# Optimization experiments

Hardware: AMD Instinct MI355X
Metric: run time of the kernel (lower is better)

The kernel has to match this reference:

```python
import jax, jax.numpy as jnp
import numpy as np

BIG = 1e30  # finite stand-in for +inf to keep grads clean


def _chamfer_loss(bin_center, ground_truth):
    # bin_center: [B, n_bins, 1] 1-D 'point cloud' of bin centers
    # ground_truth: [B, 1, H, W] depth map
    B = bin_center.shape[0]
    c = bin_center[..., 0]                      # [B, nb]
    p = ground_truth.reshape(B, -1)             # [B, V] flattened depth points
    mask = p >= 0.001                           # valid (non-near-zero) depths
    n = jnp.sum(mask, axis=1)                   # [B] valid count per sample
    Lmax = jnp.max(n)                           # pad_sequence pads every sample to L_max
    npad = (Lmax - n).astype(c.dtype)           # number of zero pad-points per sample

    # pairwise squared distances between bin centers and depth points
    D = (c[:, :, None] - p[:, None, :]) ** 2    # [B, nb, V]

    # direction 1: gt points -> nearest bin center (sum over points)
    dmin_p = jnp.min(D, axis=1)                 # [B, V]
    sumA = jnp.sum(jnp.where(mask, dmin_p, 0.0), axis=1)
    # each zero pad-point contributes min_j c_j^2
    c2 = c ** 2                                 # [B, nb]
    sumA = sumA + npad * jnp.min(c2, axis=1)

    # direction 2: bin centers -> nearest gt point (incl. zero pad-points if any)
    Dm = jnp.where(mask[:, None, :], D, jnp.asarray(BIG, D.dtype))
    min_valid = jnp.min(Dm, axis=2)             # [B, nb] min over valid points
    has_pad = (npad > 0)[:, None]
    min_b = jnp.where(has_pad, jnp.minimum(min_valid, c2), min_valid)
    sumB = jnp.sum(min_b, axis=1)               # [B]

    # chamferdist: point_reduction=sum, batch_reduction=mean, bidirectional
    return jnp.mean(sumA + sumB)


def setup_inputs() -> dict:
    key = jax.random.key(0)
    k1, k2 = jax.random.split(key)
    bin_center = jax.random.uniform(k1, (4, 256, 1), dtype=jnp.float32)
    ground_truth = jax.random.uniform(k2, (4, 1, 352, 448), dtype=jnp.float32)
    return {"bin_center": bin_center, "ground_truth": ground_truth}


def reference(bin_center, ground_truth):
    return _chamfer_loss(bin_center, ground_truth)
```

## Files before the change

### kernel.cpp

```cpp
#include <hip/hip_runtime.h>

#define NB   256
#define TPB  256
#define NI   (NB + 1)
#define G    128
#define MINF 1e30f
#define CAPD 1e15f

__global__ __launch_bounds__(NB) void k_sort(const float* __restrict__ bc,
                                             float* __restrict__ sbins,
                                             unsigned* __restrict__ gmin,
                                             unsigned* __restrict__ gmax) {
    __shared__ float s[NB];
    const int tid = threadIdx.x, b = blockIdx.x;
    s[tid] = bc[b * NB + tid];
    for (int t = tid; t < NI; t += NB) {
        gmin[b * NI + t] = 0xFFFFFFFFu;
        gmax[b * NI + t] = 0u;
    }
    __syncthreads();
    for (int k = 2; k <= NB; k <<= 1)
        for (int j = k >> 1; j > 0; j >>= 1) {
            const int ixj = tid ^ j;
            if (ixj > tid) {
                const float a = s[tid], bv = s[ixj];
                if ((a > bv) == ((tid & k) == 0)) { s[tid] = bv; s[ixj] = a; }
            }
            __syncthreads();
        }
    sbins[b * NB + tid] = s[tid];
}

__global__ __launch_bounds__(TPB) void k_main(
    const float* __restrict__ sbins, const float* __restrict__ gt,
    int V, int CH,
    float* __restrict__ sumA_part, int* __restrict__ cnt_part,
    unsigned* __restrict__ gmin, unsigned* __restrict__ gmax)
{
    const int b   = blockIdx.x / G;
    const int blk = blockIdx.x % G;
    const int tid = threadIdx.x;
    const int start = blk * CH;
    const int cn = min(CH, V - start);
    const float* __restrict__ gp = gt + (size_t)b * V + start;

    __shared__ float    c[NB];
    __shared__ unsigned imn[NI], imx[NI];
    c[tid] = sbins[b * NB + tid];
    for (int t = tid; t < NI; t += TPB) { imn[t] = 0xFFFFFFFFu; imx[t] = 0u; }
    __syncthreads();

    float sum = 0.f; int cnt = 0;
    for (int i = tid; i < cn; i += TPB) {
        const float q = gp[i];
        if (q >= 0.001f) {
            int idx = 0;
            #pragma unroll
            for (int st = 128; st >= 1; st >>= 1)
                idx += (c[idx + st - 1] <= q) ? st : 0;
            idx += (c[idx] <= q) ? 1 : 0;
            const float dlo = (idx > 0)  ? (q - c[idx - 1]) : MINF;
            const float dhi = (idx < NB) ? (c[idx] - q)     : MINF;
            const float d = fminf(dlo, dhi);
            sum += d * d; ++cnt;
            atomicMin(&imn[idx], __float_as_uint(q));
            atomicMax(&imx[idx], __float_as_uint(q));
        }
    }
    __syncthreads();

    for (int t = tid; t < NI; t += TPB) {
        const unsigned lo = imn[t], hi = imx[t];
        if (lo != 0xFFFFFFFFu) atomicMin(&gmin[b * NI + t], lo);
        if (hi != 0u)          atomicMax(&gmax[b * NI + t], hi);
    }

    for (int off = 32; off; off >>= 1) {
        sum += __shfl_down(sum, off);
        cnt += __shfl_down(cnt, off);
    }
    __shared__ float r4[4]; __shared__ int i4[4];
    if ((tid & 63) == 0) { r4[tid >> 6] = sum; i4[tid >> 6] = cnt; }
    __syncthreads();
    if (tid == 0) {
        sumA_part[blockIdx.x] = r4[0] + r4[1] + r4[2] + r4[3];
        cnt_part [blockIdx.x] = i4[0] + i4[1] + i4[2] + i4[3];
    }
}

__global__ __launch_bounds__(TPB) void k_final(
    const float* __restrict__ sbins,
    const float* __restrict__ sumA_part, const int* __restrict__ cnt_part,
    const unsigned* __restrict__ gmin, const unsigned* __restrict__ gmax,
    int B, float* __restrict__ out)
{
    const int tid = threadIdx.x;
    __shared__ float pm[NB], sm[NB];
    __shared__ float r4[4]; __shared__ int i4[4]; __shared__ float q4[4];
    __shared__ float ssa[8]; __shared__ int sn[8];

    for (int bb = 0; bb < B; ++bb) {
        float s = 0.f; int cc = 0;
        for (int k = tid; k < G; k += TPB) {
            s  += sumA_part[bb * G + k];
            cc += cnt_part [bb * G + k];
        }
        for (int off = 32; off; off >>= 1) { s += __shfl_down(s, off); cc += __shfl_down(cc, off); }
        if ((tid & 63) == 0) { r4[tid >> 6] = s; i4[tid >> 6] = cc; }
        __syncthreads();
        if (tid == 0) { ssa[bb] = r4[0]+r4[1]+r4[2]+r4[3]; sn[bb] = i4[0]+i4[1]+i4[2]+i4[3]; }
        __syncthreads();
    }
    int Lmax = 0;
    for (int bb = 0; bb < B; ++bb) Lmax = max(Lmax, sn[bb]);

    float total = 0.f;
    for (int bb = 0; bb < B; ++bb) {
        const unsigned hib = gmax[bb * NI + tid];
        const unsigned lob = gmin[bb * NI + tid + 1];
        pm[tid] = (hib == 0u)          ? -MINF : __uint_as_float(hib);
        sm[tid] = (lob == 0xFFFFFFFFu) ?  MINF : __uint_as_float(lob);
        __syncthreads();
        for (int off = 1; off < NB; off <<= 1) {
            const float vp = pm[tid], vs = sm[tid];
            const float op = (tid >= off)     ? pm[tid - off] : -MINF;
            const float os = (tid + off < NB) ? sm[tid + off] :  MINF;
            __syncthreads();
            pm[tid] = fmaxf(vp, op);
            sm[tid] = fminf(vs, os);
            __syncthreads();
        }
        const float cj = sbins[bb * NB + tid];
        const float c2 = cj * cj;
        const float d  = fminf(fminf(cj - pm[tid], sm[tid] - cj), CAPD);
        float bm = d * d;
        const int npad = Lmax - sn[bb];
        if (npad > 0) bm = fminf(bm, c2);
        float s = bm, mc = c2;
        for (int off = 32; off; off >>= 1) {
            s  += __shfl_down(s, off);
            mc  = fminf(mc, __shfl_down(mc, off));
        }
        if ((tid & 63) == 0) { r4[tid >> 6] = s; q4[tid >> 6] = mc; }
        __syncthreads();
        if (tid == 0)
            total += ssa[bb]
                   + (float)npad * fminf(fminf(q4[0], q4[1]), fminf(q4[2], q4[3]))
                   + (r4[0] + r4[1] + r4[2] + r4[3]);
        __syncthreads();
    }
    if (tid == 0) out[0] = total / (float)B;
}

extern "C" void kernel_launch(void* const* d_in, const int* in_sizes, int n_in,
                              void* d_out, int out_size, void* d_ws, size_t ws_size,
                              hipStream_t stream) {
    const float* bc = (const float*)d_in[0];
    const float* gt = (const float*)d_in[1];
    const int B  = in_sizes[0] / NB;
    const int V  = in_sizes[1] / B;
    const int CH = (V + G - 1) / G;

    float*    sbins     = (float*)d_ws;
    float*    sumA_part = sbins + (size_t)B * NB;
    int*      cnt_part  = (int*)(sumA_part + (size_t)B * G);
    unsigned* gmin      = (unsigned*)(cnt_part + (size_t)B * G);
    unsigned* gmax      = gmin + (size_t)B * NI;

    k_sort <<<B, NB, 0, stream>>>(bc, sbins, gmin, gmax);
    k_main <<<B * G, TPB, 0, stream>>>(sbins, gt, V, CH,
                                       sumA_part, cnt_part, gmin, gmax);
    k_final<<<1, TPB, 0, stream>>>(sbins, sumA_part, cnt_part,
                                   gmin, gmax, B, (float*)d_out);
}
```

Measured before the change: 79.94 us.

## Fuse sort, main and final kernels into one launch with last-block reduction

Merges the three kernels into one. Every block sorts its own copy of the bin centers in shared memory, and the last block to finish, found with a global atomic counter, runs the final reduction. The shared-memory prefix max/min scan in the final stage becomes wave shuffles plus a small cross-wave combine. Two memsets now handle the initialisation. This removes launch gaps and the serialized tiny sort and final kernels, at the cost of redundant per-block bitonic sorts and two extra memset operations.

```diff
diff --git a/kernel.cpp b/kernel.cpp
--- a/kernel.cpp
+++ b/kernel.cpp
@@ -7,48 +7,40 @@
 #define MINF 1e30f
 #define CAPD 1e15f
 
-__global__ __launch_bounds__(NB) void k_sort(const float* __restrict__ bc,
-                                             float* __restrict__ sbins,
-                                             unsigned* __restrict__ gmin,
-                                             unsigned* __restrict__ gmax) {
-    __shared__ float s[NB];
-    const int tid = threadIdx.x, b = blockIdx.x;
-    s[tid] = bc[b * NB + tid];
-    for (int t = tid; t < NI; t += NB) {
-        gmin[b * NI + t] = 0xFFFFFFFFu;
-        gmax[b * NI + t] = 0u;
-    }
+__global__ __launch_bounds__(TPB, 2) void k_all(
+    const float* __restrict__ bc, const float* __restrict__ gt,
+    int V, int CH, int B,
+    float* __restrict__ sumA_part, int* __restrict__ cnt_part,
+    unsigned* __restrict__ gmin, unsigned* __restrict__ gmax,
+    float* __restrict__ sbins, unsigned* __restrict__ counter,
+    float* __restrict__ out)
+{
+    const int tid  = threadIdx.x;
+    const int b    = blockIdx.x / G;
+    const int blk  = blockIdx.x % G;
+    const int lane = tid & 63, w = tid >> 6;
+
+    __shared__ float    c[NB];
+    __shared__ unsigned imn[NI], imx[NI];
+    __shared__ float r4[4]; __shared__ int i4[4];
+
+    c[tid] = bc[b * NB + tid];
+    for (int t = tid; t < NI; t += TPB) { imn[t] = 0xFFFFFFFFu; imx[t] = 0u; }
     __syncthreads();
     for (int k = 2; k <= NB; k <<= 1)
         for (int j = k >> 1; j > 0; j >>= 1) {
             const int ixj = tid ^ j;
             if (ixj > tid) {
-                const float a = s[tid], bv = s[ixj];
-                if ((a > bv) == ((tid & k) == 0)) { s[tid] = bv; s[ixj] = a; }
+                const float a = c[tid], bv = c[ixj];
+                if ((a > bv) == ((tid & k) == 0)) { c[tid] = bv; c[ixj] = a; }
             }
             __syncthreads();
         }
-    sbins[b * NB + tid] = s[tid];
-}
+    if (blk == 0) sbins[b * NB + tid] = c[tid];
 
-__global__ __launch_bounds__(TPB) void k_main(
-    const float* __restrict__ sbins, const float* __restrict__ gt,
-    int V, int CH,
-    float* __restrict__ sumA_part, int* __restrict__ cnt_part,
-    unsigned* __restrict__ gmin, unsigned* __restrict__ gmax)
-{
-    const int b   = blockIdx.x / G;
-    const int blk = blockIdx.x % G;
-    const int tid = threadIdx.x;
     const int start = blk * CH;
     const int cn = min(CH, V - start);
     const float* __restrict__ gp = gt + (size_t)b * V + start;
-
-    __shared__ float    c[NB];
-    __shared__ unsigned imn[NI], imx[NI];
-    c[tid] = sbins[b * NB + tid];
-    for (int t = tid; t < NI; t += TPB) { imn[t] = 0xFFFFFFFFu; imx[t] = 0u; }
-    __syncthreads();
 
     float sum = 0.f; int cnt = 0;
     for (int i = tid; i < cn; i += TPB) {
@@ -79,25 +71,23 @@
         sum += __shfl_down(sum, off);
         cnt += __shfl_down(cnt, off);
     }
-    __shared__ float r4[4]; __shared__ int i4[4];
-    if ((tid & 63) == 0) { r4[tid >> 6] = sum; i4[tid >> 6] = cnt; }
+    if (lane == 0) { r4[w] = sum; i4[w] = cnt; }
     __syncthreads();
     if (tid == 0) {
         sumA_part[blockIdx.x] = r4[0] + r4[1] + r4[2] + r4[3];
         cnt_part [blockIdx.x] = i4[0] + i4[1] + i4[2] + i4[3];
     }
-}
 
-__global__ __launch_bounds__(TPB) void k_final(
-    const float* __restrict__ sbins,
-    const float* __restrict__ sumA_part, const int* __restrict__ cnt_part,
-    const unsigned* __restrict__ gmin, const unsigned* __restrict__ gmax,
-    int B, float* __restrict__ out)
-{
-    const int tid = threadIdx.x;
-    __shared__ float pm[NB], sm[NB];
-    __shared__ float r4[4]; __shared__ int i4[4]; __shared__ float q4[4];
+    __threadfence();
+    __syncthreads();
+    __shared__ int lastFlag;
+    if (tid == 0) lastFlag = (atomicAdd(counter, 1u) == (unsigned)(gridDim.x - 1));
+    __syncthreads();
+    if (!lastFlag) return;
+    __threadfence();
+
     __shared__ float ssa[8]; __shared__ int sn[8];
+    __shared__ float wtop[4], wbot[4], q4[4];
 
     for (int bb = 0; bb < B; ++bb) {
         float s = 0.f; int cc = 0;
@@ -106,7 +96,7 @@
             cc += cnt_part [bb * G + k];
         }
         for (int off = 32; off; off >>= 1) { s += __shfl_down(s, off); cc += __shfl_down(cc, off); }
-        if ((tid & 63) == 0) { r4[tid >> 6] = s; i4[tid >> 6] = cc; }
+        if (lane == 0) { r4[w] = s; i4[w] = cc; }
         __syncthreads();
         if (tid == 0) { ssa[bb] = r4[0]+r4[1]+r4[2]+r4[3]; sn[bb] = i4[0]+i4[1]+i4[2]+i4[3]; }
         __syncthreads();
@@ -118,21 +108,31 @@
     for (int bb = 0; bb < B; ++bb) {
         const unsigned hib = gmax[bb * NI + tid];
         const unsigned lob = gmin[bb * NI + tid + 1];
-        pm[tid] = (hib == 0u)          ? -MINF : __uint_as_float(hib);
-        sm[tid] = (lob == 0xFFFFFFFFu) ?  MINF : __uint_as_float(lob);
+        float pv = (hib == 0u)          ? -MINF : __uint_as_float(hib);
+        float sv = (lob == 0xFFFFFFFFu) ?  MINF : __uint_as_float(lob);
+
+        #pragma unroll
+        for (int off = 1; off < 64; off <<= 1) {
+            const float o = __shfl_up(pv, off);
+            if (lane >= off) pv = fmaxf(pv, o);
+        }
+        #pragma unroll
+        for (int off = 1; off < 64; off <<= 1) {
+            const float o = __shfl_down(sv, off);
+            if (lane < 64 - off) sv = fminf(sv, o);
+        }
+        if (lane == 63) wtop[w] = pv;
+        if (lane == 0)  wbot[w] = sv;
         __syncthreads();
-        for (int off = 1; off < NB; off <<= 1) {
-            const float vp = pm[tid], vs = sm[tid];
-            const float op = (tid >= off)     ? pm[tid - off] : -MINF;
-            const float os = (tid + off < NB) ? sm[tid + off] :  MINF;
-            __syncthreads();
-            pm[tid] = fmaxf(vp, op);
-            sm[tid] = fminf(vs, os);
-            __syncthreads();
+        #pragma unroll
+        for (int ww = 0; ww < 4; ++ww) {
+            if (ww < w) pv = fmaxf(pv, wtop[ww]);
+            if (ww > w) sv = fminf(sv, wbot[ww]);
         }
+
         const float cj = sbins[bb * NB + tid];
         const float c2 = cj * cj;
-        const float d  = fminf(fminf(cj - pm[tid], sm[tid] - cj), CAPD);
+        const float d  = fminf(fminf(cj - pv, sv - cj), CAPD);
         float bm = d * d;
         const int npad = Lmax - sn[bb];
         if (npad > 0) bm = fminf(bm, c2);
@@ -141,7 +141,7 @@
             s  += __shfl_down(s, off);
             mc  = fminf(mc, __shfl_down(mc, off));
         }
-        if ((tid & 63) == 0) { r4[tid >> 6] = s; q4[tid >> 6] = mc; }
+        if (lane == 0) { r4[w] = s; q4[w] = mc; }
         __syncthreads();
         if (tid == 0)
             total += ssa[bb]
@@ -166,10 +166,13 @@
     int*      cnt_part  = (int*)(sumA_part + (size_t)B * G);
     unsigned* gmin      = (unsigned*)(cnt_part + (size_t)B * G);
     unsigned* gmax      = gmin + (size_t)B * NI;
+    unsigned* counter   = gmax + (size_t)B * NI;
 
-    k_sort <<<B, NB, 0, stream>>>(bc, sbins, gmin, gmax);
-    k_main <<<B * G, TPB, 0, stream>>>(sbins, gt, V, CH,
-                                       sumA_part, cnt_part, gmin, gmax);
-    k_final<<<1, TPB, 0, stream>>>(sbins, sumA_part, cnt_part,
-                                   gmin, gmax, B, (float*)d_out);
+    hipMemsetAsync(gmin, 0xFF, (size_t)B * NI * sizeof(unsigned), stream);
+    hipMemsetAsync(gmax, 0x00, (size_t)B * NI * sizeof(unsigned) + sizeof(unsigned),
+                   stream);
+
+    k_all<<<B * G, TPB, 0, stream>>>(bc, gt, V, CH, B,
+                                     sumA_part, cnt_part, gmin, gmax,
+                                     sbins, counter, (float*)d_out);
 }
```

After: 108.1 us. +35.2%, slower.
